# Kernel optimization log

Hardware: AMD Instinct MI355X
Metric: run time of the kernel (lower is better)

## Reference

```python
import jax, jax.numpy as jnp
import numpy as np
from jax import lax

B, N, K, NCP = 4, 2048, 20, 400
EPS = 1e-5


def _bn(x, gamma, beta, axes):
    # training-mode batch norm (biased variance), channel axis = 1
    m = jnp.mean(x, axis=axes, keepdims=True)
    v = jnp.var(x, axis=axes, keepdims=True)
    shape = [1] * x.ndim
    shape[1] = -1
    return (x - m) * lax.rsqrt(v + EPS) * gamma.reshape(shape) + beta.reshape(shape)


def _knn_idx(x, k):
    # x: [B, C, N] -> idx [B, N, k] (nearest, includes self like torch.cdist+topk(largest=False))
    x2 = jnp.sum(x * x, axis=1)  # [B, N]
    d = x2[:, :, None] + x2[:, None, :] - 2.0 * jnp.einsum('bcn,bcm->bnm', x, x)
    return lax.top_k(-d, k)[1]


def _edge_conv(x, w, gamma, beta, k):
    # x: [B, C, N], w: [O, 2C] -> [B, O, N] (1x1 conv + BN + LeakyReLU + max over k)
    idx = _knn_idx(x, k)                      # [B, N, k]
    xt = jnp.transpose(x, (0, 2, 1))          # [B, N, C]
    b = jnp.arange(xt.shape[0])[:, None, None]
    nbr = xt[b, idx]                          # [B, N, k, C]
    ctr = xt[:, :, None, :]
    feat = jnp.concatenate([nbr - ctr, jnp.broadcast_to(ctr, nbr.shape)], axis=-1)  # [B, N, k, 2C]
    y = jnp.einsum('bnkc,oc->bonk', feat, w)  # [B, O, N, k]
    y = jax.nn.leaky_relu(_bn(y, gamma, beta, axes=(0, 2, 3)), 0.2)
    return jnp.max(y, axis=-1)                # [B, O, N]


def setup_inputs() -> dict:
    key = jax.random.key(0)
    ks = jax.random.split(key, 16)
    rnd = lambda k_, s: jax.random.normal(k_, s, dtype=jnp.float32) * 0.02
    inp = {
        'x': jax.random.normal(ks[0], (B, 3, N), dtype=jnp.float32),
        'w1': rnd(ks[1], (64, 6)),    'g1': jnp.ones(64),   'b1': jnp.zeros(64),
        'w2': rnd(ks[2], (128, 128)), 'g2': jnp.ones(128),  'b2': jnp.zeros(128),
        'w3': rnd(ks[3], (256, 256)), 'g3': jnp.ones(256),  'b3': jnp.zeros(256),
        'w4': rnd(ks[4], (512, 512)), 'g4': jnp.ones(512),  'b4': jnp.zeros(512),
        'w5': rnd(ks[5], (2048, 963)), 'g5': jnp.ones(2048), 'b5': jnp.zeros(2048),
        'w6': rnd(ks[6], (2048, 2048)), 'wb6': jnp.zeros(2048), 'g6': jnp.ones(2048), 'b6': jnp.zeros(2048),
        'w7': rnd(ks[7], (4096, 4096)), 'wb7': jnp.zeros(4096), 'g7': jnp.ones(4096), 'b7': jnp.zeros(4096),
        'w8': rnd(ks[8], (NCP, 4096)), 'wb8': jnp.zeros(NCP),
    }
    return inp


def reference(x, w1, g1, b1, w2, g2, b2, w3, g3, b3, w4, g4, b4,
              w5, g5, b5, w6, wb6, g6, b6, w7, wb7, g7, b7, w8, wb8):
    x0 = x                                            # [B, 3, N]
    x1 = _edge_conv(x0, w1, g1, b1, K)                # [B, 64, N]
    x2 = _edge_conv(x1, w2, g2, b2, K)                # [B, 128, N]
    x3 = _edge_conv(x2, w3, g3, b3, K)                # [B, 256, N]
    x4 = _edge_conv(x3, w4, g4, b4, K)                # [B, 512, N]
    h = jnp.concatenate([x0, x1, x2, x3, x4], axis=1) # [B, 963, N]
    h = jnp.einsum('bcn,oc->bon', h, w5)              # [B, 2048, N]
    h = jax.nn.leaky_relu(_bn(h, g5, b5, axes=(0, 2)), 0.2)
    p = jnp.max(h, axis=-1, keepdims=True)            # [B, 2048, 1] global max pool
    y = jnp.einsum('bcl,oc->bol', p, w6) + wb6[None, :, None]
    y = jax.nn.relu(_bn(y, g6, b6, axes=(0, 2)))
    y = jnp.concatenate([y, p], axis=1)               # [B, 4096, 1]
    y = jnp.einsum('bcl,oc->bol', y, w7) + wb7[None, :, None]
    y = jax.nn.relu(_bn(y, g7, b7, axes=(0, 2)))
    y = jnp.einsum('bcl,oc->bol', y, w8) + wb8[None, :, None]
    return jnp.tanh(y[:, :, 0])                       # [B, NCP]
```

## Files before the change

### kernel.cpp

```cpp
#include <hip/hip_runtime.h>
#include <float.h>
#include <math.h>


#define NPTS 2048
#define BATCH 4
#define KNN 20
#define CH_H 963
#define KPAD 992
#define HSTRIDE (CH_H*NPTS)

typedef _Float16 half8 __attribute__((ext_vector_type(8)));
typedef float f32x4 __attribute__((ext_vector_type(4)));

__device__ __forceinline__ unsigned fenc(float x){
  unsigned u = __float_as_uint(x);
  return (u & 0x80000000u) ? ~u : (u | 0x80000000u);
}
__device__ __forceinline__ float fdec(unsigned u){
  u = (u & 0x80000000u) ? (u ^ 0x80000000u) : ~u;
  return __uint_as_float(u);
}

__global__ void k_convert(const float* __restrict__ x, float* __restrict__ H){
  int i = blockIdx.x*256 + threadIdx.x;
  if (i >= BATCH*3*NPTS) return;
  int b = i / (3*NPTS); int r = i % (3*NPTS);
  H[(size_t)b*HSTRIDE + r] = x[i];
}

__global__ void k_norms(const float* __restrict__ X, int C, float* __restrict__ X2,
                        float* __restrict__ SUMZ){
  int i = blockIdx.x*256 + threadIdx.x;
  if (i < 1024) SUMZ[i] = 0.f;
  int b = i >> 11, n = i & 2047;
  const float* Xb = X + (size_t)b*HSTRIDE + n;
  float s = 0.f;
  for (int c=0;c<C;++c){ float v = Xb[(size_t)c*NPTS]; s = fmaf(v,v,s); }
  X2[i] = s;
}

__global__ __launch_bounds__(256) void k_xsplit(const float* __restrict__ X, int C, int Cpad,
        _Float16* __restrict__ Xhi, _Float16* __restrict__ Xlo)
{
  __shared__ float t[64][65];
  int b = blockIdx.z;
  int n0 = blockIdx.x*64, c0 = blockIdx.y*64;
  int tid = threadIdx.x; int l = tid & 63, m = tid >> 6;
  for (int cc = m; cc < 64; cc += 4){
    int c = c0 + cc;
    t[cc][l] = (c < C) ? X[(size_t)b*HSTRIDE + (size_t)c*NPTS + n0 + l] : 0.f;
  }
  __syncthreads();
  for (int nn = m; nn < 64; nn += 4){
    int c = c0 + l;
    if (c < Cpad){
      float v = t[l][nn];
      _Float16 h = (_Float16)v;
      size_t o = ((size_t)(b<<11)+n0+nn)*Cpad + c;
      Xhi[o] = h;
      Xlo[o] = (_Float16)(v - (float)h);
    }
  }
}

__global__ __launch_bounds__(256) void k_gram(const _Float16* __restrict__ Xhi,
        const _Float16* __restrict__ Xlo, int Cpad, int bbase,
        float* __restrict__ G0, float* __restrict__ G1)
{
  __shared__ half8 AsH[128][4]; __shared__ half8 AsL[128][4];
  __shared__ half8 BsH[128][4]; __shared__ half8 BsL[128][4];
  int bl = blockIdx.z;
  int b  = bbase + bl;
  float* G = bl ? G1 : G0;
  const _Float16* Hb = Xhi + (size_t)(b<<11)*Cpad;
  const _Float16* Lb = Xlo + (size_t)(b<<11)*Cpad;
  int m0 = blockIdx.x*128, n0 = blockIdx.y*128;
  int tid = threadIdx.x;
  int w = tid>>6, lane = tid&63;
  int wm = w>>1, wn = w&1;
  int quad = lane>>4, col = lane&15;
  f32x4 acc[4][4];
  #pragma unroll
  for (int i=0;i<4;++i)
    #pragma unroll
    for (int j=0;j<4;++j) acc[i][j] = (f32x4){0.f,0.f,0.f,0.f};

  for (int k0=0; k0<Cpad; k0+=32){
    #pragma unroll
    for (int h=0; h<2; ++h){
      int cid = tid + h*256;
      int row = cid>>2, kc = cid&3;
      size_t ao = (size_t)(n0+row)*Cpad + k0 + kc*8;
      size_t bo = (size_t)(m0+row)*Cpad + k0 + kc*8;
      AsH[row][kc] = *(const half8*)(Hb + ao);
      AsL[row][kc] = *(const half8*)(Lb + ao);
      BsH[row][kc] = *(const half8*)(Hb + bo);
      BsL[row][kc] = *(const half8*)(Lb + bo);
    }
    __syncthreads();
    half8 ah[4], al[4], bh[4], blo[4];
    #pragma unroll
    for (int mt=0;mt<4;++mt){ ah[mt] = AsH[wm*64 + mt*16 + col][quad];
                              al[mt] = AsL[wm*64 + mt*16 + col][quad]; }
    #pragma unroll
    for (int nt=0;nt<4;++nt){ bh[nt] = BsH[wn*64 + nt*16 + col][quad];
                              blo[nt] = BsL[wn*64 + nt*16 + col][quad]; }
    #pragma unroll
    for (int mt=0;mt<4;++mt)
      #pragma unroll
      for (int nt=0;nt<4;++nt){
        acc[mt][nt] = __builtin_amdgcn_mfma_f32_16x16x32_f16(ah[mt], bh[nt], acc[mt][nt], 0, 0, 0);
        acc[mt][nt] = __builtin_amdgcn_mfma_f32_16x16x32_f16(ah[mt], blo[nt], acc[mt][nt], 0, 0, 0);
        acc[mt][nt] = __builtin_amdgcn_mfma_f32_16x16x32_f16(al[mt], bh[nt], acc[mt][nt], 0, 0, 0);
      }
    __syncthreads();
  }
  #pragma unroll
  for (int mt=0;mt<4;++mt){
    #pragma unroll
    for (int r=0;r<4;++r){
      int n = n0 + wm*64 + mt*16 + quad*4 + r;
      #pragma unroll
      for (int nt=0;nt<4;++nt){
        int m = m0 + wn*64 + nt*16 + col;
        G[(size_t)n*2048 + m] = acc[mt][nt][r];
      }
    }
  }
}

#define KNN_CH(OPC) OPC(0) OPC(1) OPC(2) OPC(3) OPC(4) OPC(5) OPC(6) OPC(7)
#define DECL_CH(ch) float d##ch##_0,d##ch##_1,d##ch##_2,d##ch##_3;
#define LOADG_CH(ch) { float4 g = *(const float4*)(grow + (ch)*256 + base); \
  float4 xm = *(const float4*)(x2b + (ch)*256 + base); \
  d##ch##_0 = x2n + xm.x - 2.f*g.x; d##ch##_1 = x2n + xm.y - 2.f*g.y; \
  d##ch##_2 = x2n + xm.z - 2.f*g.z; d##ch##_3 = x2n + xm.w - 2.f*g.w; }
#define DECL_G(ch) float gv##ch; int gm##ch;
#define MKCH(ch) { gv##ch = d##ch##_0; gm##ch = (ch)*256 + base; \
  if (d##ch##_1 < gv##ch){ gv##ch = d##ch##_1; gm##ch = (ch)*256 + base + 1; } \
  if (d##ch##_2 < gv##ch){ gv##ch = d##ch##_2; gm##ch = (ch)*256 + base + 2; } \
  if (d##ch##_3 < gv##ch){ gv##ch = d##ch##_3; gm##ch = (ch)*256 + base + 3; } }
#define REMCASE(ch) case ch: { \
  if (own){ if (cp==0) d##ch##_0 = FLT_MAX; else if (cp==1) d##ch##_1 = FLT_MAX; \
            else if (cp==2) d##ch##_2 = FLT_MAX; else d##ch##_3 = FLT_MAX; } \
  MKCH(ch) } break;

__global__ __launch_bounds__(256,4) void k_sel(const float* __restrict__ G0,
        const float* __restrict__ G1, const float* __restrict__ X2,
        int bbase, int* __restrict__ IDX)
{
  int tid = threadIdx.x;
  int w = tid >> 6, lane = tid & 63;
  int n = blockIdx.x*4 + w;
  int b = bbase + blockIdx.y;
  const float* grow = (blockIdx.y ? G1 : G0) + (size_t)n*2048;
  const float* x2b  = X2 + (b<<11);
  float x2n = x2b[n];
  int base = lane << 2;
  KNN_CH(DECL_CH)
  KNN_CH(LOADG_CH)
  KNN_CH(DECL_G)
  KNN_CH(MKCH)
  int* op = IDX + ((size_t)(b<<11)+n)*KNN;
  for (int it=0; it<KNN; ++it){
    float v = fminf(fminf(fminf(gv0,gv1),fminf(gv2,gv3)),
                    fminf(fminf(gv4,gv5),fminf(gv6,gv7)));
    #pragma unroll
    for (int s=1; s<64; s<<=1) v = fminf(v, __shfl_xor(v, s));
    int mc = 0x7fffffff;
    mc = (gv7==v) ? gm7 : mc;
    mc = (gv6==v) ? gm6 : mc;
    mc = (gv5==v) ? gm5 : mc;
    mc = (gv4==v) ? gm4 : mc;
    mc = (gv3==v) ? gm3 : mc;
    mc = (gv2==v) ? gm2 : mc;
    mc = (gv1==v) ? gm1 : mc;
    mc = (gv0==v) ? gm0 : mc;
    int m = mc;
    #pragma unroll
    for (int s=1; s<64; s<<=1) m = min(m, __shfl_xor(m, s));
    if (lane==0) op[it] = m;
    int sm = __builtin_amdgcn_readfirstlane(m);
    bool own = (lane == ((sm>>2)&63));
    int cp = sm & 3;
    switch (sm >> 8){ KNN_CH(REMCASE) }
  }
}

__global__ __launch_bounds__(256) void k_vu(const float* __restrict__ X,
        const float* __restrict__ W, int C, int O,
        float* __restrict__ V, float* __restrict__ U)
{
  __shared__ float Xs[8][128];
  __shared__ float Wdv[8][64];
  __shared__ float Wuv[8][64];
  int b = blockIdx.z, n0 = blockIdx.x*128, o0 = blockIdx.y*64;
  int tid = threadIdx.x;
  int tj = tid & 15, ti = tid >> 4;
  float4 aV[8], aU[8];
  #pragma unroll
  for (int i=0;i<8;++i){ aV[i]=make_float4(0,0,0,0); aU[i]=make_float4(0,0,0,0); }
  const float* Xb = X + (size_t)b*HSTRIDE;
  for (int c0=0;c0<C;c0+=8){
    {
      int cc = tid >> 5, nn = (tid & 31) * 4; int c = c0 + cc;
      float4 v = (c<C) ? *(const float4*)(Xb + (size_t)c*NPTS + n0 + nn)
                       : make_float4(0,0,0,0);
      *(float4*)&Xs[cc][nn] = v;
    }
    for (int l=tid;l<512;l+=256){
      int oo=l>>3, cc=l&7, c=c0+cc;
      float wd=0.f, wu=0.f;
      if (c<C){
        const float* wr = W + (size_t)(o0+oo)*(2*C);
        wd = wr[c]; wu = wr[C+c] - wd;
      }
      Wdv[cc][oo]=wd; Wuv[cc][oo]=wu;
    }
    __syncthreads();
    #pragma unroll
    for (int cc=0;cc<8;++cc){
      float4 x0 = *(float4*)&Xs[cc][ti*8];
      float4 x1 = *(float4*)&Xs[cc][ti*8+4];
      float4 wd = *(float4*)&Wdv[cc][tj*4];
      float4 wu = *(float4*)&Wuv[cc][tj*4];
      float xs[8] = {x0.x,x0.y,x0.z,x0.w,x1.x,x1.y,x1.z,x1.w};
      #pragma unroll
      for (int i=0;i<8;++i){
        aV[i].x = fmaf(xs[i], wd.x, aV[i].x);
        aV[i].y = fmaf(xs[i], wd.y, aV[i].y);
        aV[i].z = fmaf(xs[i], wd.z, aV[i].z);
        aV[i].w = fmaf(xs[i], wd.w, aV[i].w);
        aU[i].x = fmaf(xs[i], wu.x, aU[i].x);
        aU[i].y = fmaf(xs[i], wu.y, aU[i].y);
        aU[i].z = fmaf(xs[i], wu.z, aU[i].z);
        aU[i].w = fmaf(xs[i], wu.w, aU[i].w);
      }
    }
    __syncthreads();
  }
  #pragma unroll
  for (int i=0;i<8;++i){
    int n = n0 + ti*8 + i;
    size_t basep = ((size_t)b*NPTS + n)*O + o0 + tj*4;
    *(float4*)(V+basep) = aV[i];
    *(float4*)(U+basep) = aU[i];
  }
}

__global__ __launch_bounds__(256) void k_gather(const float* __restrict__ V, const float* __restrict__ U,
        const int* __restrict__ IDX, int O,
        float* __restrict__ YMX, float* __restrict__ YMN,
        float* __restrict__ SUM, float* __restrict__ SUMSQ)
{
  const int NT = 8;
  __shared__ int sidx[NT*KNN];
  int bi = blockIdx.x;
  int b  = bi >> 8;
  int n0 = (bi & 255) * NT;
  int tid = threadIdx.x;
  for (int l = tid; l < NT*KNN; l += 256)
    sidx[l] = IDX[((size_t)(b<<11)+n0)*KNN + l];
  __syncthreads();
  int othr  = (O < 256) ? O : 256;
  int o0    = tid & (othr-1);
  int ns    = tid / othr;
  int nstep = 256 / othr;
  for (int o = o0; o < O; o += othr){
    float s = 0.f, q = 0.f;
    for (int nn = ns; nn < NT; nn += nstep){
      int n = n0 + nn;
      size_t ub = ((size_t)(b<<11)+n)*O + o;
      float u = U[ub];
      float mx = -FLT_MAX, mn = FLT_MAX;
      #pragma unroll
      for (int k=0;k<KNN;++k){
        int m = sidx[nn*KNN+k];
        float y = V[((size_t)(b<<11)+m)*O + o] + u;
        mx = fmaxf(mx,y); mn = fminf(mn,y);
        s += y; q = fmaf(y,y,q);
      }
      YMX[ub] = mx; YMN[ub] = mn;
    }
    atomicAdd(&SUM[o], s); atomicAdd(&SUMSQ[o], q);
  }
}

__global__ void k_finalize(const float* __restrict__ SUM, const float* __restrict__ SUMSQ,
        const float* __restrict__ g, const float* __restrict__ bt,
        int O, float invM, float* __restrict__ SC, float* __restrict__ SH){
  int o = blockIdx.x*256 + threadIdx.x;
  if (o>=O) return;
  float m = SUM[o]*invM;
  float var = SUMSQ[o]*invM - m*m;
  float sc = g[o] * rsqrtf(var + 1e-5f);
  SC[o]=sc; SH[o] = bt[o] - m*sc;
}

__global__ __launch_bounds__(256) void k_apply(const float* __restrict__ YMX, const float* __restrict__ YMN,
        const float* __restrict__ SC, const float* __restrict__ SH,
        int O, float* __restrict__ OUT)
{
  __shared__ float t[64][65];
  int b = blockIdx.z;
  int o0 = blockIdx.y*64, n0 = blockIdx.x*64;
  int tid = threadIdx.x;
  int lo = tid & 63, ln = tid >> 6;
  float sc = SC[o0+lo], sh = SH[o0+lo];
  for (int nn = ln; nn < 64; nn += 4){
    size_t idx = ((size_t)(b<<11)+n0+nn)*O + o0 + lo;
    float v = (sc >= 0.f) ? YMX[idx] : YMN[idx];
    float y = fmaf(sc, v, sh);
    y = (y > 0.f) ? y : 0.2f*y;
    t[lo][nn] = y;
  }
  __syncthreads();
  for (int oo = ln; oo < 64; oo += 4){
    OUT[(size_t)b*HSTRIDE + (size_t)(o0+oo)*NPTS + n0 + lo] = t[oo][lo];
  }
}

__global__ __launch_bounds__(256) void k_h2f16(const float* __restrict__ H, _Float16* __restrict__ Hf){
  __shared__ float t[64][65];
  int b = blockIdx.z;
  int n0 = blockIdx.x*64, c0 = blockIdx.y*64;
  int tid = threadIdx.x; int l = tid & 63, m = tid >> 6;
  for (int cc = m; cc < 64; cc += 4){
    int c = c0 + cc;
    t[cc][l] = (c < CH_H) ? H[(size_t)b*HSTRIDE + (size_t)c*NPTS + n0 + l] : 0.f;
  }
  __syncthreads();
  for (int nn = m; nn < 64; nn += 4){
    int c = c0 + l;
    if (c < KPAD)
      Hf[((size_t)(b<<11)+n0+nn)*KPAD + c] = (_Float16)t[l][nn];
  }
}

__global__ void k_w5f16(const float* __restrict__ w5, _Float16* __restrict__ Wf,
                        unsigned* __restrict__ z){
  int i = blockIdx.x*256 + threadIdx.x;
  if (i < 12288) z[i] = 0u;
  else if (i < 20480) z[i] = 0xFFFFFFFFu;
  if (i >= 2048*KPAD) return;
  int o = i / KPAD, c = i - o*KPAD;
  Wf[i] = (c < CH_H) ? (_Float16)w5[(size_t)o*CH_H + c] : (_Float16)0.f;
}

__global__ __launch_bounds__(256) void k_l5mfma(const _Float16* __restrict__ Wf,
        const _Float16* __restrict__ Hf,
        float* __restrict__ SUM5, float* __restrict__ SUMSQ5,
        unsigned* __restrict__ MAXB, unsigned* __restrict__ MINB)
{
  __shared__ half8 As[128][4];
  __shared__ half8 Bs[128][4];
  int b  = blockIdx.z;
  int n0 = blockIdx.x*128, o0 = blockIdx.y*128;
  int tid = threadIdx.x;
  int w = tid>>6, lane = tid&63;
  int wm = w>>1, wn = w&1;
  int quad = lane>>4, col = lane&15;
  f32x4 acc[4][4];
  #pragma unroll
  for (int i=0;i<4;++i)
    #pragma unroll
    for (int j=0;j<4;++j) acc[i][j] = (f32x4){0.f,0.f,0.f,0.f};

  for (int k0=0; k0<KPAD; k0+=32){
    #pragma unroll
    for (int h=0; h<2; ++h){
      int cid = tid + h*256;
      int row = cid>>2, kc = cid&3;
      As[row][kc] = *(const half8*)(Wf + (size_t)(o0+row)*KPAD + k0 + kc*8);
      Bs[row][kc] = *(const half8*)(Hf + ((size_t)(b<<11)+n0+row)*KPAD + k0 + kc*8);
    }
    __syncthreads();
    half8 af[4], bf[4];
    #pragma unroll
    for (int mt=0;mt<4;++mt) af[mt] = As[wm*64 + mt*16 + col][quad];
    #pragma unroll
    for (int nt=0;nt<4;++nt) bf[nt] = Bs[wn*64 + nt*16 + col][quad];
    #pragma unroll
    for (int mt=0;mt<4;++mt)
      #pragma unroll
      for (int nt=0;nt<4;++nt)
        acc[mt][nt] = __builtin_amdgcn_mfma_f32_16x16x32_f16(af[mt], bf[nt], acc[mt][nt], 0, 0, 0);
    __syncthreads();
  }
  #pragma unroll
  for (int mt=0;mt<4;++mt){
    #pragma unroll
    for (int r=0;r<4;++r){
      float s=0.f, q=0.f, mx=-FLT_MAX, mn=FLT_MAX;
      #pragma unroll
      for (int nt=0;nt<4;++nt){
        float y = acc[mt][nt][r];
        s += y; q = fmaf(y,y,q);
        mx = fmaxf(mx,y); mn = fminf(mn,y);
      }
      #pragma unroll
      for (int d=8; d; d>>=1){
        s += __shfl_down(s,(unsigned)d,16);
        q += __shfl_down(q,(unsigned)d,16);
        mx = fmaxf(mx,__shfl_down(mx,(unsigned)d,16));
        mn = fminf(mn,__shfl_down(mn,(unsigned)d,16));
      }
      if (col==0){
        int o = o0 + wm*64 + mt*16 + quad*4 + r;
        atomicAdd(&SUM5[o], s);
        atomicAdd(&SUMSQ5[o], q);
        atomicMax(&MAXB[(b<<11)+o], fenc(mx));
        atomicMin(&MINB[(b<<11)+o], fenc(mn));
      }
    }
  }
}

__global__ void k_l5_final(const float* __restrict__ SUM5, const float* __restrict__ SUMSQ5,
        const unsigned* __restrict__ MAXB, const unsigned* __restrict__ MINB,
        const float* __restrict__ g5, const float* __restrict__ b5, float* __restrict__ P)
{
  int o = blockIdx.x*256 + threadIdx.x;
  if (o>=2048) return;
  float m = SUM5[o]*(1.f/8192.f);
  float var = SUMSQ5[o]*(1.f/8192.f) - m*m;
  float sc = g5[o] * rsqrtf(var + 1e-5f);
  float sh = b5[o] - m*sc;
  for (int b=0;b<4;++b){
    float mx = fdec(MAXB[b*2048+o]);
    float mn = fdec(MINB[b*2048+o]);
    float v = (sc >= 0.f) ? fmaf(sc,mx,sh) : fmaf(sc,mn,sh);
    v = (v > 0.f) ? v : 0.2f*v;
    P[b*2048 + o] = v;
  }
}

__global__ __launch_bounds__(256) void k_fc(const float* __restrict__ W, const float* __restrict__ bias,
        const float* __restrict__ Z, int Cin, int O, float* __restrict__ Y)
{
  int o = blockIdx.x*4 + (threadIdx.x>>6);
  int lane = threadIdx.x & 63;
  if (o >= O) return;
  const float* wr = W + (size_t)o*Cin;
  float a0=0.f,a1=0.f,a2=0.f,a3=0.f;
  for (int c=lane;c<Cin;c+=64){
    float w = wr[c];
    a0 = fmaf(w, Z[c],        a0);
    a1 = fmaf(w, Z[Cin+c],    a1);
    a2 = fmaf(w, Z[2*Cin+c],  a2);
    a3 = fmaf(w, Z[3*Cin+c],  a3);
  }
  #pragma unroll
  for (int s=32;s;s>>=1){
    a0 += __shfl_down(a0,(unsigned)s); a1 += __shfl_down(a1,(unsigned)s);
    a2 += __shfl_down(a2,(unsigned)s); a3 += __shfl_down(a3,(unsigned)s);
  }
  if (lane==0){
    float bb = bias[o];
    Y[o]=a0+bb; Y[O+o]=a1+bb; Y[2*O+o]=a2+bb; Y[3*O+o]=a3+bb;
  }
}

__global__ void k_bn4(const float* __restrict__ Y, const float* __restrict__ g, const float* __restrict__ bt,
                      int O, float* __restrict__ Z, int zstride, int zoff)
{
  int o = blockIdx.x*256 + threadIdx.x;
  if (o>=O) return;
  float v0=Y[o], v1=Y[O+o], v2=Y[2*O+o], v3=Y[3*O+o];
  float m = 0.25f*(v0+v1+v2+v3);
  float d0=v0-m, d1=v1-m, d2=v2-m, d3=v3-m;
  float var = 0.25f*(d0*d0+d1*d1+d2*d2+d3*d3);
  float sc = g[o] * rsqrtf(var + 1e-5f);
  float sh = bt[o] - m*sc;
  Z[0*zstride+zoff+o] = fmaxf(fmaf(sc,v0,sh), 0.f);
  Z[1*zstride+zoff+o] = fmaxf(fmaf(sc,v1,sh), 0.f);
  Z[2*zstride+zoff+o] = fmaxf(fmaf(sc,v2,sh), 0.f);
  Z[3*zstride+zoff+o] = fmaxf(fmaf(sc,v3,sh), 0.f);
}

__global__ void k_copy_p(const float* __restrict__ P, float* __restrict__ Z){
  int i = blockIdx.x*256 + threadIdx.x;
  int b = i>>11, o = i&2047;
  Z[b*4096 + 2048 + o] = P[i];
}

__global__ __launch_bounds__(256) void k_final(const float* __restrict__ W8, const float* __restrict__ wb8,
        const float* __restrict__ Z7, float* __restrict__ out)
{
  int o = blockIdx.x*4 + (threadIdx.x>>6);
  int lane = threadIdx.x & 63;
  if (o >= 400) return;
  const float* wr = W8 + (size_t)o*4096;
  float a0=0.f,a1=0.f,a2=0.f,a3=0.f;
  for (int c=lane;c<4096;c+=64){
    float w = wr[c];
    a0 = fmaf(w, Z7[c],        a0);
    a1 = fmaf(w, Z7[4096+c],   a1);
    a2 = fmaf(w, Z7[2*4096+c], a2);
    a3 = fmaf(w, Z7[3*4096+c], a3);
  }
  #pragma unroll
  for (int s=32;s;s>>=1){
    a0 += __shfl_down(a0,(unsigned)s); a1 += __shfl_down(a1,(unsigned)s);
    a2 += __shfl_down(a2,(unsigned)s); a3 += __shfl_down(a3,(unsigned)s);
  }
  if (lane==0){
    float bb = wb8[o];
    out[0*400+o] = tanhf(a0+bb);
    out[1*400+o] = tanhf(a1+bb);
    out[2*400+o] = tanhf(a2+bb);
    out[3*400+o] = tanhf(a3+bb);
  }
}

extern "C" void kernel_launch(void* const* d_in, const int* in_sizes, int n_in,
                              void* d_out, int out_size, void* d_ws, size_t ws_size,
                              hipStream_t stream)
{
  const float* x   = (const float*)d_in[0];
  const float* w_e[4]  = {(const float*)d_in[1], (const float*)d_in[4], (const float*)d_in[7], (const float*)d_in[10]};
  const float* g_e[4]  = {(const float*)d_in[2], (const float*)d_in[5], (const float*)d_in[8], (const float*)d_in[11]};
  const float* b_e[4]  = {(const float*)d_in[3], (const float*)d_in[6], (const float*)d_in[9], (const float*)d_in[12]};
  const float* w5  = (const float*)d_in[13];
  const float* g5  = (const float*)d_in[14];
  const float* b5  = (const float*)d_in[15];
  const float* w6  = (const float*)d_in[16];
  const float* wb6 = (const float*)d_in[17];
  const float* g6  = (const float*)d_in[18];
  const float* b6  = (const float*)d_in[19];
  const float* w7  = (const float*)d_in[20];
  const float* wb7 = (const float*)d_in[21];
  const float* g7  = (const float*)d_in[22];
  const float* b7  = (const float*)d_in[23];
  const float* w8  = (const float*)d_in[24];
  const float* wb8 = (const float*)d_in[25];

  float* WS = (float*)d_ws;
  float* H    = WS;
  float* V    = WS + 7888896;
  float* U    = V  + 4194304;
  float* YMX  = U  + 4194304;
  float* YMN  = YMX+ 4194304;
  int*   IDX  = (int*)(YMN + 4194304);
  float* X2   = (float*)(IDX + 163840);
  float* SUM  = X2 + 8192;
  float* SUMSQ= SUM + 512;
  float* SC   = SUMSQ + 512;
  float* SH   = SC + 512;
  float* SUM5 = SH + 512;
  float* SUMSQ5 = SUM5 + 2048;
  unsigned* MAXB = (unsigned*)(SUMSQ5 + 2048);
  unsigned* MINB = MAXB + 8192;
  float* P    = (float*)(MINB + 8192);
  float* Y6   = P + 8192;
  float* Z    = Y6 + 8192;
  float* Y7   = Z + 16384;
  float* Z7   = Y7 + 16384;
  _Float16* Hf  = (_Float16*)V;
  _Float16* Wf  = (_Float16*)U;
  _Float16* Xhi = (_Float16*)U;
  _Float16* Xlo = (_Float16*)U + 4*2048*256;
  float* G0 = YMX;
  float* G1 = YMN;

  k_convert<<<96,256,0,stream>>>(x, H);

  const int Cin_[4]  = {3,64,128,256};
  const int Cpad_[4] = {32,64,128,256};
  const int O_[4]    = {64,128,256,512};
  const int ioff_[4] = {0,3,67,195};
  const int ooff_[4] = {3,67,195,451};

  for (int l=0;l<4;++l){
    const float* Xl = H + (size_t)ioff_[l]*NPTS;
    int C = Cin_[l], Cpad = Cpad_[l], O = O_[l];
    k_norms<<<32,256,0,stream>>>(Xl, C, X2, SUM);
    dim3 gxs(32, (Cpad+63)/64, 4);
    k_xsplit<<<gxs,256,0,stream>>>(Xl, C, Cpad, Xhi, Xlo);
    dim3 ggr(16,16,2);
    k_gram<<<ggr,256,0,stream>>>(Xhi, Xlo, Cpad, 0, G0, G1);
    dim3 gsl(512,2);
    k_sel<<<gsl,256,0,stream>>>(G0, G1, X2, 0, IDX);
    k_gram<<<ggr,256,0,stream>>>(Xhi, Xlo, Cpad, 2, G0, G1);
    k_sel<<<gsl,256,0,stream>>>(G0, G1, X2, 2, IDX);
    dim3 gvu(16, O/64, 4);
    k_vu<<<gvu,256,0,stream>>>(Xl, w_e[l], C, O, V, U);
    k_gather<<<1024,256,0,stream>>>(V, U, IDX, O, YMX, YMN, SUM, SUMSQ);
    k_finalize<<<2,256,0,stream>>>(SUM, SUMSQ, g_e[l], b_e[l], O, 1.f/163840.f, SC, SH);
    dim3 gap(32, O/64, 4);
    k_apply<<<gap,256,0,stream>>>(YMX, YMN, SC, SH, O, H + (size_t)ooff_[l]*NPTS);
  }

  dim3 gtr(32,16,4);
  k_h2f16<<<gtr,256,0,stream>>>(H, Hf);
  k_w5f16<<<(2048*KPAD+255)/256,256,0,stream>>>(w5, Wf, (unsigned*)SUM5);
  dim3 g5g(16,16,4);
  k_l5mfma<<<g5g,256,0,stream>>>(Wf, Hf, SUM5, SUMSQ5, MAXB, MINB);
  k_l5_final<<<8,256,0,stream>>>(SUM5, SUMSQ5, MAXB, MINB, g5, b5, P);

  k_fc<<<512,256,0,stream>>>(w6, wb6, P, 2048, 2048, Y6);
  k_bn4<<<8,256,0,stream>>>(Y6, g6, b6, 2048, Z, 4096, 0);
  k_copy_p<<<32,256,0,stream>>>(P, Z);
  k_fc<<<1024,256,0,stream>>>(w7, wb7, Z, 4096, 4096, Y7);
  k_bn4<<<16,256,0,stream>>>(Y7, g7, b7, 4096, Z7, 4096, 0);
  k_final<<<100,256,0,stream>>>(w8, wb8, Z7, (float*)d_out);
}
```

Baseline: 1.194 ms.

## Template gather kernel with XCD-aware block mapping and block-reduced BN stats

Rewrites the edge-conv gather kernel as a template over channel chunk size. Blocks are remapped so each XCD (bid&7) handles one batch half, which keeps the gathered V rows local to that XCD's L2. Larger layers are split into 128-channel chunks across more blocks. Per-point statistics are computed algebraically from the V sums plus the U terms, which moves the U add out of the k loop. Partial sums are reduced in shared memory before one atomic per channel per block, and U and the outputs use nontemporal accesses. The risks are a mapping that depends on the hardware scheduler's round-robin assignment to XCDs, and small numerical differences from the algebraic variance expansion.

```diff
diff --git a/kernel.cpp b/kernel.cpp
--- a/kernel.cpp
+++ b/kernel.cpp
@@ -249,41 +249,60 @@
   }
 }
 
-__global__ __launch_bounds__(256) void k_gather(const float* __restrict__ V, const float* __restrict__ U,
-        const int* __restrict__ IDX, int O,
+template<int OC, int CHN>
+__global__ __launch_bounds__(256) void k_gather(const float* __restrict__ V,
+        const float* __restrict__ U, const int* __restrict__ IDX,
         float* __restrict__ YMX, float* __restrict__ YMN,
         float* __restrict__ SUM, float* __restrict__ SUMSQ)
 {
-  const int NT = 8;
+  constexpr int O = OC*CHN;
+  constexpr int NT = 8;
+  constexpr int NSTEP = 256/OC;
   __shared__ int sidx[NT*KNN];
-  int bi = blockIdx.x;
-  int b  = bi >> 8;
-  int n0 = (bi & 255) * NT;
+  __shared__ float rs[256], rq[256];
+  int bid = blockIdx.x;
+  int xcd  = bid & 7;
+  int b    = xcd >> 1;
+  int half = xcd & 1;
+  int r    = bid >> 3;
+  int ngrp, chunk;
+  if (CHN == 1){ ngrp = (half<<7) | r; chunk = 0; }
+  else         { ngrp = r & 255; chunk = half*(CHN/2) + (r>>8); }
+  int n0 = ngrp * NT;
   int tid = threadIdx.x;
   for (int l = tid; l < NT*KNN; l += 256)
     sidx[l] = IDX[((size_t)(b<<11)+n0)*KNN + l];
   __syncthreads();
-  int othr  = (O < 256) ? O : 256;
-  int o0    = tid & (othr-1);
-  int ns    = tid / othr;
-  int nstep = 256 / othr;
-  for (int o = o0; o < O; o += othr){
-    float s = 0.f, q = 0.f;
-    for (int nn = ns; nn < NT; nn += nstep){
-      int n = n0 + nn;
-      size_t ub = ((size_t)(b<<11)+n)*O + o;
-      float u = U[ub];
-      float mx = -FLT_MAX, mn = FLT_MAX;
-      #pragma unroll
-      for (int k=0;k<KNN;++k){
-        int m = sidx[nn*KNN+k];
-        float y = V[((size_t)(b<<11)+m)*O + o] + u;
-        mx = fmaxf(mx,y); mn = fminf(mn,y);
-        s += y; q = fmaf(y,y,q);
-      }
-      YMX[ub] = mx; YMN[ub] = mn;
-    }
-    atomicAdd(&SUM[o], s); atomicAdd(&SUMSQ[o], q);
+  int o  = chunk*OC + (tid & (OC-1));
+  int ns = tid / OC;
+  const float* Vb = V + (size_t)(b<<11)*O + o;
+  float s = 0.f, q = 0.f;
+  #pragma unroll
+  for (int i = 0; i < NT/NSTEP; ++i){
+    int nn = ns + i*NSTEP;
+    int n = n0 + nn;
+    size_t ub = ((size_t)(b<<11)+n)*O + o;
+    float sv = 0.f, sv2 = 0.f, mx = -FLT_MAX, mn = FLT_MAX;
+    #pragma unroll
+    for (int k=0;k<KNN;++k){
+      int m = sidx[nn*KNN+k];
+      float v = Vb[(size_t)m*O];
+      mx = fmaxf(mx,v); mn = fminf(mn,v);
+      sv += v; sv2 = fmaf(v,v,sv2);
+    }
+    float u = __builtin_nontemporal_load(U + ub);
+    __builtin_nontemporal_store(mx + u, YMX + ub);
+    __builtin_nontemporal_store(mn + u, YMN + ub);
+    s += sv + (float)KNN * u;
+    q += sv2 + 2.f*u*sv + (float)KNN*u*u;
+  }
+  rs[tid] = s; rq[tid] = q;
+  __syncthreads();
+  if (tid < OC){
+    #pragma unroll
+    for (int t=1; t<NSTEP; ++t){ s += rs[tid + t*OC]; q += rq[tid + t*OC]; }
+    atomicAdd(&SUM[o], s);
+    atomicAdd(&SUMSQ[o], q);
   }
 }
 
@@ -586,7 +605,14 @@
     k_sel<<<gsl,256,0,stream>>>(G0, G1, X2, 2, IDX);
     dim3 gvu(16, O/64, 4);
     k_vu<<<gvu,256,0,stream>>>(Xl, w_e[l], C, O, V, U);
-    k_gather<<<1024,256,0,stream>>>(V, U, IDX, O, YMX, YMN, SUM, SUMSQ);
+    if (O == 64)
+      k_gather<64,1><<<1024,256,0,stream>>>(V, U, IDX, YMX, YMN, SUM, SUMSQ);
+    else if (O == 128)
+      k_gather<128,1><<<1024,256,0,stream>>>(V, U, IDX, YMX, YMN, SUM, SUMSQ);
+    else if (O == 256)
+      k_gather<128,2><<<2048,256,0,stream>>>(V, U, IDX, YMX, YMN, SUM, SUMSQ);
+    else
+      k_gather<128,4><<<4096,256,0,stream>>>(V, U, IDX, YMX, YMN, SUM, SUMSQ);
     k_finalize<<<2,256,0,stream>>>(SUM, SUMSQ, g_e[l], b_e[l], O, 1.f/163840.f, SC, SH);
     dim3 gap(32, O/64, 4);
     k_apply<<<gap,256,0,stream>>>(YMX, YMN, SC, SH, O, H + (size_t)ooff_[l]*NPTS);
```

Result: faster. 1.081 ms (-9.5%).
